# Kernel tuning notes

Hardware: AMD Instinct MI355X
Metric: run time of the kernel (lower is better)

The kernel has to match this reference:

```python
import math
import jax, jax.numpy as jnp
import numpy as np

B, N, F, K = 4, 4096, 128, 32
EPS = 1e-8  # tsl.epsilon
TEMP0, TEMP_DECAY = 1.0, 0.99995


def setup_inputs() -> dict:
    key = jax.random.key(0)
    k1, k2, k3, k4 = jax.random.split(key, 4)
    emb = jax.random.normal(k1, (B, N, F), dtype=jnp.float32)
    adj = jax.random.uniform(k2, (B, N, N), dtype=jnp.float32)
    logits_param = jax.random.normal(k3, (N, K), dtype=jnp.float32)
    u = jax.random.uniform(k4, (B, N, K), dtype=jnp.float32, minval=1e-9, maxval=1.0)
    gumbel_noise = -jnp.log(-jnp.log(u))
    return {"emb": emb, "adj": adj, "logits_param": logits_param, "gumbel_noise": gumbel_noise}


def reference(emb, adj, logits_param, gumbel_noise):
    # temp decays on each get_temp() call in training mode (called twice per forward)
    t1 = max(TEMP0 * TEMP_DECAY, 0.05)
    t2 = max(t1 * TEMP_DECAY, 0.05)

    # ---- gumbel-softmax hard sample with straight-through estimator ----
    y_soft = jax.nn.softmax(logits_param[None] / t1 + gumbel_noise, axis=-1)  # [B,N,K]
    y_hard = jax.nn.one_hot(jnp.argmax(y_soft, axis=-1), K, dtype=y_soft.dtype)
    s_sample = jax.lax.stop_gradient(y_hard - y_soft) + y_soft + EPS  # [B,N,K]

    # ---- soft assignment for regularizers (unbatched [N,K]) ----
    s_soft = jax.nn.softmax(logits_param / t2, axis=-1)  # [N,K]

    # mincut_num = trace(s^T A s) per batch, without forming [K,K]
    As = jnp.einsum('bnm,mk->bnk', adj, s_soft)            # [B,N,K]
    mincut_num = jnp.einsum('nk,bnk->b', s_soft, As)       # [B]
    # mincut_den = trace(s^T D s): D is diag(deg) -> O(N*K) instead of diag_embed
    d_flat = adj.sum(axis=-1)                              # [B,N]
    mincut_den = jnp.einsum('bn,nk,nk->b', d_flat, s_soft, s_soft)
    mincut_loss = -jnp.mean(mincut_num / mincut_den)

    ss = s_soft.T @ s_soft                                 # [K,K]
    ortho_loss = jnp.linalg.norm(ss / jnp.linalg.norm(ss) - jnp.eye(K, dtype=ss.dtype) / math.sqrt(K))

    # ---- pooling ----
    out_emb = jnp.einsum('bnk,bnf->bkf', s_sample, emb)    # [B,K,F]
    As2 = jnp.einsum('bnm,bml->bnl', adj, s_sample)        # [B,N,K]
    out_adj = jnp.einsum('bnk,bnl->bkl', s_sample, As2)    # [B,K,K]

    out_adj = out_adj * (1.0 - jnp.eye(K, dtype=out_adj.dtype))  # zero diagonal
    d = jnp.sqrt(out_adj.sum(axis=-1, keepdims=True)) + EPS
    out_adj = out_adj / d / jnp.swapaxes(d, -1, -2)

    return out_emb, out_adj, s_sample, mincut_loss, ortho_loss
```

## Files before the change

### kernel.cpp

```cpp
#include <hip/hip_runtime.h>
#include <hip/hip_bf16.h>
#include <math.h>

#define B_ 4
#define N_ 4096
#define F_ 128
#define K_ 32
#define EPS_ 1e-8f

typedef __attribute__((ext_vector_type(8))) __bf16 bf16x8;
typedef __attribute__((ext_vector_type(4))) float f32x4;

#define WS_SSOFT   0
#define WS_SQ      131072
#define WS_SS      135168
#define WS_WFS     136192
#define WS_WFH     201728
#define WS_OADJP   463872
#define WS_NUMDEN  1512448
#define WS_PEMB    1514496
#define WS_OADJ    2563072
#define WS_H       2567168

__global__ void k_pre(const float* __restrict__ logits, const float* __restrict__ gum,
                      float* __restrict__ s_soft, float* __restrict__ sq,
                      float* __restrict__ ss, float* __restrict__ s_sample,
                      int* __restrict__ h, bf16x8* __restrict__ wfs,
                      bf16x8* __restrict__ wfh, float t1, float t2) {
  __shared__ float sl[64][33];
  __shared__ int hl[4][64];
  int t = threadIdx.x;
  int r = blockIdx.x;
  int n0 = r * 64;

  if (t < 64) {
    int n = n0 + t;
    float z[32];
    float mx = -1e30f;
    for (int k = 0; k < 32; ++k) { z[k] = logits[n*32+k] / t2; mx = fmaxf(mx, z[k]); }
    float s = 0.f;
    for (int k = 0; k < 32; ++k) { z[k] = expf(z[k]-mx); s += z[k]; }
    float sqa = 0.f;
    for (int k = 0; k < 32; ++k) {
      float v = z[k] / s;
      s_soft[n*32+k] = v;
      sl[t][k] = v;
      sqa += v*v;
    }
    sq[n] = sqa;
  }

  {
    int b = t >> 6, nn = t & 63;
    int n = n0 + nn;
    size_t i = (size_t)b * N_ + n;
    float z[32];
    float mx = -1e30f;
    for (int k = 0; k < 32; ++k) { z[k] = logits[n*32+k]/t1 + gum[i*32+k]; mx = fmaxf(mx, z[k]); }
    float s = 0.f;
    for (int k = 0; k < 32; ++k) { z[k] = expf(z[k]-mx); s += z[k]; }
    int am = 0; float best = -1.f;
    for (int k = 0; k < 32; ++k) { z[k] = z[k]/s; if (z[k] > best) { best = z[k]; am = k; } }
    for (int k = 0; k < 32; ++k) {
      float yh = (k==am) ? 1.f : 0.f;
      s_sample[i*32+k] = (yh - z[k]) + z[k] + EPS_;
    }
    h[i] = am;
    hl[b][nn] = am;
  }
  __syncthreads();

  for (int pp = 0; pp < 4; ++pp) {
    int p = pp*256 + t;
    int k = p >> 5, l = p & 31;
    float a = 0.f;
    for (int rr = 0; rr < 64; ++rr) a += sl[rr][k]*sl[rr][l];
    atomicAdd(&ss[p], a);
  }

  {
    int lane = t & 63;
    int c = (t >> 6) & 1;
    int tts = t >> 7;
    int col = c*16 + (lane & 15);
    int lrow = tts*32 + (lane >> 4)*8;
    bf16x8 v;
    #pragma unroll
    for (int j = 0; j < 8; ++j) v[j] = (__bf16)sl[lrow+j][col];
    wfs[((size_t)(2*r + tts)*2 + c)*64 + lane] = v;
  }

  for (int it = 0; it < 4; ++it) {
    int p = it*256 + t;
    int lane = p & 63;
    int c = (p >> 6) & 1;
    int tts = (p >> 7) & 1;
    int b = p >> 8;
    int cc = c*16 + (lane & 15);
    int lrow = tts*32 + (lane >> 4)*8;
    bf16x8 v;
    #pragma unroll
    for (int j = 0; j < 8; ++j) v[j] = (__bf16)((hl[b][lrow+j] == cc) ? 1.f : 0.f);
    wfh[(((size_t)b*(N_/32) + 2*r + tts)*2 + c)*64 + lane] = v;
  }
}

#define NT(p) __builtin_nontemporal_load((const f32x4*)(p))

__launch_bounds__(256, 4)
__global__ void k_gemm(const float* __restrict__ adj, const bf16x8* __restrict__ wfs,
                       const bf16x8* __restrict__ wfh,
                       const float* __restrict__ s_soft, const float* __restrict__ sq,
                       const int* __restrict__ h, float* __restrict__ numden_p,
                       float* __restrict__ oadjp) {
  __shared__ float oal[1024];
  __shared__ float rn[4], rd[4];
  int t = threadIdx.x;
  int w = t >> 6, l = t & 63;
  int lr = l & 15, lhi = l >> 4;
  int bid = blockIdx.x;
  int sp = bid & 7, r = (bid >> 3) & 31, b = bid >> 8;

  for (int i = t; i < 1024; i += 256) oal[i] = 0.f;
  __syncthreads();

  int row0 = r*128;
  int m0 = sp*512;
  int rowA = row0 + w*32 + lr;

  const float* pA0 = adj + (size_t)b*N_*N_ + (size_t)rowA*N_ + m0 + lhi*8;
  const float* pA1 = pA0 + (size_t)16*N_;
  const bf16x8* pws = wfs + (size_t)(m0 >> 5)*128 + l;
  const bf16x8* pwh = wfh + ((size_t)b*(N_/32) + (m0 >> 5))*128 + l;

  f32x4 acc00 = {0,0,0,0}, acc01 = {0,0,0,0}, acc02 = {0,0,0,0}, acc03 = {0,0,0,0};
  f32x4 acc10 = {0,0,0,0}, acc11 = {0,0,0,0}, acc12 = {0,0,0,0}, acc13 = {0,0,0,0};

  f32x4 a0lo = NT(pA0), a0hi = NT(pA0 + 4);
  f32x4 a1lo = NT(pA1), a1hi = NT(pA1 + 4);
  bf16x8 wc0 = pws[0], wc1 = pws[64], wc2 = pwh[0], wc3 = pwh[64];

  #pragma unroll 1
  for (int c = 0; c < 16; ++c) {
    f32x4 n0lo, n0hi, n1lo, n1hi;
    bf16x8 wn0, wn1, wn2, wn3;
    if (c < 15) {
      pA0 += 32; pA1 += 32; pws += 128; pwh += 128;
      n0lo = NT(pA0); n0hi = NT(pA0 + 4);
      n1lo = NT(pA1); n1hi = NT(pA1 + 4);
      wn0 = pws[0]; wn1 = pws[64]; wn2 = pwh[0]; wn3 = pwh[64];
    }
    bf16x8 fa0, fa1;
    #pragma unroll
    for (int j = 0; j < 4; ++j) {
      fa0[j]   = (__bf16)a0lo[j];
      fa0[j+4] = (__bf16)a0hi[j];
      fa1[j]   = (__bf16)a1lo[j];
      fa1[j+4] = (__bf16)a1hi[j];
    }
    acc00 = __builtin_amdgcn_mfma_f32_16x16x32_bf16(fa0, wc0, acc00, 0, 0, 0);
    acc01 = __builtin_amdgcn_mfma_f32_16x16x32_bf16(fa0, wc1, acc01, 0, 0, 0);
    acc02 = __builtin_amdgcn_mfma_f32_16x16x32_bf16(fa0, wc2, acc02, 0, 0, 0);
    acc03 = __builtin_amdgcn_mfma_f32_16x16x32_bf16(fa0, wc3, acc03, 0, 0, 0);
    acc10 = __builtin_amdgcn_mfma_f32_16x16x32_bf16(fa1, wc0, acc10, 0, 0, 0);
    acc11 = __builtin_amdgcn_mfma_f32_16x16x32_bf16(fa1, wc1, acc11, 0, 0, 0);
    acc12 = __builtin_amdgcn_mfma_f32_16x16x32_bf16(fa1, wc2, acc12, 0, 0, 0);
    acc13 = __builtin_amdgcn_mfma_f32_16x16x32_bf16(fa1, wc3, acc13, 0, 0, 0);
    if (c < 15) {
      a0lo = n0lo; a0hi = n0hi; a1lo = n1lo; a1hi = n1hi;
      wc0 = wn0; wc1 = wn1; wc2 = wn2; wc3 = wn3;
    }
  }

  float numacc = 0.f, denacc = 0.f;
  {
    f32x4 a0s[2] = {acc00, acc10}, a1s[2] = {acc01, acc11};
    f32x4 a2s[2] = {acc02, acc12}, a3s[2] = {acc03, acc13};
    int wrow0 = row0 + w*32;
    #pragma unroll
    for (int rt = 0; rt < 2; ++rt) {
      int rbase = wrow0 + rt*16 + lhi*4;
      #pragma unroll
      for (int i = 0; i < 4; ++i) {
        int row = rbase + i;
        float sqv = sq[row];
        int hv = h[b*N_ + row];
        numacc += a0s[rt][i] * s_soft[row*32 + lr];
        numacc += a1s[rt][i] * s_soft[row*32 + 16 + lr];
        float v2 = a2s[rt][i], v3 = a3s[rt][i];
        denacc += (v2 + v3) * sqv;
        atomicAdd(&oal[hv*32 + lr], v2);
        atomicAdd(&oal[hv*32 + 16 + lr], v3);
      }
    }
  }
  for (int off = 32; off; off >>= 1) {
    numacc += __shfl_down(numacc, off);
    denacc += __shfl_down(denacc, off);
  }
  if (l == 0) { rn[w] = numacc; rd[w] = denacc; }
  __syncthreads();
  if (t == 0) {
    numden_p[bid] = rn[0]+rn[1]+rn[2]+rn[3];
    numden_p[1024 + bid] = rd[0]+rd[1]+rd[2]+rd[3];
  }
  for (int i = t; i < 1024; i += 256) oadjp[(size_t)bid*1024 + i] = oal[i];
}

__global__ void k_outemb(const float* __restrict__ emb, const int* __restrict__ h,
                         float* __restrict__ pemb) {
  __shared__ float accl[32*128];
  int t = threadIdx.x;
  for (int i = t; i < 4096; i += 256) accl[i] = 0.f;
  __syncthreads();
  int b = blockIdx.x >> 6;
  int n0 = (blockIdx.x & 63) * 64;
  int f = t & 127, rr = t >> 7;
  for (int it = 0; it < 32; ++it) {
    int n = n0 + it*2 + rr;
    float v = emb[((size_t)b*N_ + n)*F_ + f];
    int hv = h[b*N_ + n];
    atomicAdd(&accl[hv*128 + f], v);
  }
  __syncthreads();
  for (int i = t; i < 4096; i += 256) pemb[(size_t)blockIdx.x*4096 + i] = accl[i];
}

__global__ void k_reduce(const float* __restrict__ oadjp, const float* __restrict__ pemb,
                         float* __restrict__ oadj, float* __restrict__ out_emb) {
  int blk = blockIdx.x;
  if (blk < 16) {
    int i = blk*256 + threadIdx.x;
    int b = i >> 10, ii = i & 1023;
    float s = 0.f;
    const float* p = oadjp + (size_t)(b*256)*1024 + ii;
    for (int j = 0; j < 256; ++j) s += p[(size_t)j*1024];
    oadj[i] = s;
  } else {
    int i = (blk-16)*256 + threadIdx.x;
    int b = i >> 12, ii = i & 4095;
    float s = 0.f;
    const float* p = pemb + (size_t)(b*64)*4096 + ii;
    for (int j = 0; j < 64; ++j) s += p[(size_t)j*4096];
    out_emb[i] = s;
  }
}

__global__ void k_final(const float* __restrict__ numden_p, const float* __restrict__ oadj,
                        const float* __restrict__ ss, float* __restrict__ dout) {
  __shared__ float dsh[128];
  __shared__ float red[256];
  __shared__ float nd[8];
  int t = threadIdx.x;
  if (t < 8) {
    int b = t & 3;
    const float* p = numden_p + (t >> 2)*1024 + b*256;
    float s = 0.f;
    for (int j = 0; j < 256; ++j) s += p[j];
    nd[t] = s;
  }
  if (t >= 64 && t < 192) {
    int i = t - 64;
    int b = i >> 5, k = i & 31;
    float s = 0.f;
    for (int l = 0; l < 32; ++l) if (l != k) s += oadj[b*1024 + k*32 + l];
    dsh[i] = sqrtf(s) + EPS_;
  }
  __syncthreads();
  for (int i = t; i < 4096; i += 256) {
    int b = i >> 10, k = (i >> 5) & 31, l = i & 31;
    float v = (k == l) ? 0.f : oadj[i] / (dsh[b*32+k] * dsh[b*32+l]);
    dout[16384 + i] = v;
  }
  float a = 0.f;
  for (int i = t; i < 1024; i += 256) { float v = ss[i]; a += v*v; }
  red[t] = a; __syncthreads();
  for (int s2 = 128; s2; s2 >>= 1) { if (t < s2) red[t] += red[t+s2]; __syncthreads(); }
  float fro = sqrtf(red[0]);
  __syncthreads();
  float c = 0.f;
  float inv = 1.f / fro;
  float dk = (float)(1.0 / sqrt(32.0));
  for (int i = t; i < 1024; i += 256) {
    int k = i >> 5, l = i & 31;
    float v = ss[i]*inv - ((k == l) ? dk : 0.f);
    c += v*v;
  }
  red[t] = c; __syncthreads();
  for (int s2 = 128; s2; s2 >>= 1) { if (t < s2) red[t] += red[t+s2]; __syncthreads(); }
  if (t == 0) {
    dout[544769] = sqrtf(red[0]);
    float s = 0.f;
    for (int b = 0; b < 4; ++b) s += nd[b] / nd[4+b];
    dout[544768] = -s*0.25f;
  }
}

extern "C" void kernel_launch(void* const* d_in, const int* in_sizes, int n_in,
                              void* d_out, int out_size, void* d_ws, size_t ws_size,
                              hipStream_t stream) {
  const float* emb    = (const float*)d_in[0];
  const float* adj    = (const float*)d_in[1];
  const float* logits = (const float*)d_in[2];
  const float* gum    = (const float*)d_in[3];
  float* out = (float*)d_out;
  float* ws  = (float*)d_ws;

  float t1 = 0.99995f;
  float t2 = (float)(0.99995 * 0.99995);

  float* s_soft = ws + WS_SSOFT;
  float* sq     = ws + WS_SQ;
  float* ss     = ws + WS_SS;
  bf16x8* wfs   = (bf16x8*)(ws + WS_WFS);
  bf16x8* wfh   = (bf16x8*)(ws + WS_WFH);
  float* oadjp  = ws + WS_OADJP;
  float* ndp    = ws + WS_NUMDEN;
  float* pemb   = ws + WS_PEMB;
  float* oadj   = ws + WS_OADJ;
  int* hbuf     = (int*)(ws + WS_H);

  (void)hipMemsetAsync(ss, 0, 1024 * sizeof(float), stream);

  k_pre   <<<64, 256, 0, stream>>>(logits, gum, s_soft, sq, ss, out + 20480, hbuf, wfs, wfh, t1, t2);
  k_gemm  <<<1024, 256, 0, stream>>>(adj, wfs, wfh, s_soft, sq, hbuf, ndp, oadjp);
  k_outemb<<<256, 256, 0, stream>>>(emb, hbuf, pemb);
  k_reduce<<<80, 256, 0, stream>>>(oadjp, pemb, oadj, out);
  k_final <<<1, 256, 0, stream>>>(ndp, oadj, ss, out);
}
```

Measured before the change: 424.9 us.

## Fuse out_emb into gemm launch and merge reduction/final kernels

The out_emb scatter-accumulate blocks are folded into the gemm kernel as 256 extra leading blocks, and the reduce and final kernels are merged into one post kernel with per-batch blocks. The ss Gram matrix is now written as per-block partials instead of atomics, which removes the memset. This cuts the pipeline from five launches plus a memset to three and should lower launch overhead and tail serialization. The cost is larger shared memory in the gemm kernel (4096 floats), which may reduce occupancy for the gemm blocks.

```diff
diff --git a/kernel.cpp b/kernel.cpp
--- a/kernel.cpp
+++ b/kernel.cpp
@@ -13,18 +13,17 @@
 
 #define WS_SSOFT   0
 #define WS_SQ      131072
-#define WS_SS      135168
-#define WS_WFS     136192
-#define WS_WFH     201728
-#define WS_OADJP   463872
-#define WS_NUMDEN  1512448
-#define WS_PEMB    1514496
-#define WS_OADJ    2563072
-#define WS_H       2567168
+#define WS_SSP     135168
+#define WS_WFS     200704
+#define WS_WFH     266240
+#define WS_OADJP   528384
+#define WS_NUMDEN  1576960
+#define WS_PEMB    1579008
+#define WS_H       2627584
 
 __global__ void k_pre(const float* __restrict__ logits, const float* __restrict__ gum,
                       float* __restrict__ s_soft, float* __restrict__ sq,
-                      float* __restrict__ ss, float* __restrict__ s_sample,
+                      float* __restrict__ ssp, float* __restrict__ s_sample,
                       int* __restrict__ h, bf16x8* __restrict__ wfs,
                       bf16x8* __restrict__ wfh, float t1, float t2) {
   __shared__ float sl[64][33];
@@ -75,7 +74,7 @@
     int k = p >> 5, l = p & 31;
     float a = 0.f;
     for (int rr = 0; rr < 64; ++rr) a += sl[rr][k]*sl[rr][l];
-    atomicAdd(&ss[p], a);
+    ssp[(size_t)r*1024 + p] = a;
   }
 
   {
@@ -108,18 +107,38 @@
 #define NT(p) __builtin_nontemporal_load((const f32x4*)(p))
 
 __launch_bounds__(256, 4)
-__global__ void k_gemm(const float* __restrict__ adj, const bf16x8* __restrict__ wfs,
-                       const bf16x8* __restrict__ wfh,
+__global__ void k_gemm(const float* __restrict__ adj, const float* __restrict__ emb,
+                       const bf16x8* __restrict__ wfs, const bf16x8* __restrict__ wfh,
                        const float* __restrict__ s_soft, const float* __restrict__ sq,
                        const int* __restrict__ h, float* __restrict__ numden_p,
-                       float* __restrict__ oadjp) {
-  __shared__ float oal[1024];
+                       float* __restrict__ oadjp, float* __restrict__ pemb) {
+  __shared__ float sh[4096];
   __shared__ float rn[4], rd[4];
   int t = threadIdx.x;
+  int bid = blockIdx.x;
+
+  if (bid < 256) {
+    for (int i = t; i < 4096; i += 256) sh[i] = 0.f;
+    __syncthreads();
+    int b = bid >> 6;
+    int n0 = (bid & 63) * 64;
+    int f = t & 127, rr = t >> 7;
+    for (int it = 0; it < 32; ++it) {
+      int n = n0 + it*2 + rr;
+      float v = emb[((size_t)b*N_ + n)*F_ + f];
+      int hv = h[b*N_ + n];
+      atomicAdd(&sh[hv*128 + f], v);
+    }
+    __syncthreads();
+    for (int i = t; i < 4096; i += 256) pemb[(size_t)bid*4096 + i] = sh[i];
+    return;
+  }
+
+  int gid = bid - 256;
   int w = t >> 6, l = t & 63;
   int lr = l & 15, lhi = l >> 4;
-  int bid = blockIdx.x;
-  int sp = bid & 7, r = (bid >> 3) & 31, b = bid >> 8;
+  int sp = gid & 7, r = (gid >> 3) & 31, b = gid >> 8;
+  float* oal = sh;
 
   for (int i = t; i < 1024; i += 256) oal[i] = 0.f;
   __syncthreads();
@@ -201,98 +220,86 @@
   if (l == 0) { rn[w] = numacc; rd[w] = denacc; }
   __syncthreads();
   if (t == 0) {
-    numden_p[bid] = rn[0]+rn[1]+rn[2]+rn[3];
-    numden_p[1024 + bid] = rd[0]+rd[1]+rd[2]+rd[3];
-  }
-  for (int i = t; i < 1024; i += 256) oadjp[(size_t)bid*1024 + i] = oal[i];
+    numden_p[gid] = rn[0]+rn[1]+rn[2]+rn[3];
+    numden_p[1024 + gid] = rd[0]+rd[1]+rd[2]+rd[3];
+  }
+  for (int i = t; i < 1024; i += 256) oadjp[(size_t)gid*1024 + i] = oal[i];
 }
 
-__global__ void k_outemb(const float* __restrict__ emb, const int* __restrict__ h,
-                         float* __restrict__ pemb) {
-  __shared__ float accl[32*128];
+__global__ void k_post(const float* __restrict__ oadjp, const float* __restrict__ pemb,
+                       const float* __restrict__ ndp, const float* __restrict__ ssp,
+                       float* __restrict__ dout) {
+  int blk = blockIdx.x;
   int t = threadIdx.x;
-  for (int i = t; i < 4096; i += 256) accl[i] = 0.f;
-  __syncthreads();
-  int b = blockIdx.x >> 6;
-  int n0 = (blockIdx.x & 63) * 64;
-  int f = t & 127, rr = t >> 7;
-  for (int it = 0; it < 32; ++it) {
-    int n = n0 + it*2 + rr;
-    float v = emb[((size_t)b*N_ + n)*F_ + f];
-    int hv = h[b*N_ + n];
-    atomicAdd(&accl[hv*128 + f], v);
-  }
-  __syncthreads();
-  for (int i = t; i < 4096; i += 256) pemb[(size_t)blockIdx.x*4096 + i] = accl[i];
-}
-
-__global__ void k_reduce(const float* __restrict__ oadjp, const float* __restrict__ pemb,
-                         float* __restrict__ oadj, float* __restrict__ out_emb) {
-  int blk = blockIdx.x;
-  if (blk < 16) {
-    int i = blk*256 + threadIdx.x;
-    int b = i >> 10, ii = i & 1023;
-    float s = 0.f;
-    const float* p = oadjp + (size_t)(b*256)*1024 + ii;
-    for (int j = 0; j < 256; ++j) s += p[(size_t)j*1024];
-    oadj[i] = s;
-  } else {
-    int i = (blk-16)*256 + threadIdx.x;
+  if (blk < 64) {
+    int i = blk*256 + t;
     int b = i >> 12, ii = i & 4095;
     float s = 0.f;
     const float* p = pemb + (size_t)(b*64)*4096 + ii;
     for (int j = 0; j < 64; ++j) s += p[(size_t)j*4096];
-    out_emb[i] = s;
-  }
-}
-
-__global__ void k_final(const float* __restrict__ numden_p, const float* __restrict__ oadj,
-                        const float* __restrict__ ss, float* __restrict__ dout) {
-  __shared__ float dsh[128];
-  __shared__ float red[256];
-  __shared__ float nd[8];
-  int t = threadIdx.x;
-  if (t < 8) {
-    int b = t & 3;
-    const float* p = numden_p + (t >> 2)*1024 + b*256;
-    float s = 0.f;
-    for (int j = 0; j < 256; ++j) s += p[j];
-    nd[t] = s;
-  }
-  if (t >= 64 && t < 192) {
-    int i = t - 64;
-    int b = i >> 5, k = i & 31;
-    float s = 0.f;
-    for (int l = 0; l < 32; ++l) if (l != k) s += oadj[b*1024 + k*32 + l];
-    dsh[i] = sqrtf(s) + EPS_;
-  }
-  __syncthreads();
-  for (int i = t; i < 4096; i += 256) {
-    int b = i >> 10, k = (i >> 5) & 31, l = i & 31;
-    float v = (k == l) ? 0.f : oadj[i] / (dsh[b*32+k] * dsh[b*32+l]);
-    dout[16384 + i] = v;
-  }
-  float a = 0.f;
-  for (int i = t; i < 1024; i += 256) { float v = ss[i]; a += v*v; }
-  red[t] = a; __syncthreads();
-  for (int s2 = 128; s2; s2 >>= 1) { if (t < s2) red[t] += red[t+s2]; __syncthreads(); }
-  float fro = sqrtf(red[0]);
-  __syncthreads();
-  float c = 0.f;
-  float inv = 1.f / fro;
-  float dk = (float)(1.0 / sqrt(32.0));
-  for (int i = t; i < 1024; i += 256) {
-    int k = i >> 5, l = i & 31;
-    float v = ss[i]*inv - ((k == l) ? dk : 0.f);
-    c += v*v;
-  }
-  red[t] = c; __syncthreads();
-  for (int s2 = 128; s2; s2 >>= 1) { if (t < s2) red[t] += red[t+s2]; __syncthreads(); }
-  if (t == 0) {
-    dout[544769] = sqrtf(red[0]);
-    float s = 0.f;
-    for (int b = 0; b < 4; ++b) s += nd[b] / nd[4+b];
-    dout[544768] = -s*0.25f;
+    dout[i] = s;
+  } else if (blk < 68) {
+    __shared__ float oal[1024];
+    __shared__ float dsh[32];
+    int b = blk - 64;
+    float a0 = 0.f, a1 = 0.f, a2 = 0.f, a3 = 0.f;
+    const float* p = oadjp + (size_t)b*256*1024 + t;
+    for (int j = 0; j < 256; ++j) {
+      a0 += p[0]; a1 += p[256]; a2 += p[512]; a3 += p[768];
+      p += 1024;
+    }
+    oal[t] = a0; oal[t+256] = a1; oal[t+512] = a2; oal[t+768] = a3;
+    __syncthreads();
+    if (t < 32) {
+      float s = 0.f;
+      for (int l = 0; l < 32; ++l) if (l != t) s += oal[t*32+l];
+      dsh[t] = sqrtf(s) + EPS_;
+    }
+    __syncthreads();
+    for (int i = t; i < 1024; i += 256) {
+      int k = i >> 5, l = i & 31;
+      float v = (k == l) ? 0.f : oal[i] / (dsh[k] * dsh[l]);
+      dout[16384 + b*1024 + i] = v;
+    }
+  } else {
+    __shared__ float red[256];
+    __shared__ float nd[8];
+    if (t < 8) {
+      int b = t & 3;
+      const float* p = ndp + (t >> 2)*1024 + b*256;
+      float s = 0.f;
+      for (int j = 0; j < 256; ++j) s += p[j];
+      nd[t] = s;
+    }
+    float v0 = 0.f, v1 = 0.f, v2 = 0.f, v3 = 0.f;
+    for (int r = 0; r < 64; ++r) {
+      const float* p = ssp + (size_t)r*1024 + t;
+      v0 += p[0]; v1 += p[256]; v2 += p[512]; v3 += p[768];
+    }
+    float a = v0*v0 + v1*v1 + v2*v2 + v3*v3;
+    red[t] = a; __syncthreads();
+    for (int s2 = 128; s2; s2 >>= 1) { if (t < s2) red[t] += red[t+s2]; __syncthreads(); }
+    float fro = sqrtf(red[0]);
+    __syncthreads();
+    float inv = 1.f / fro;
+    float dk = (float)(1.0 / sqrt(32.0));
+    float c = 0.f;
+    {
+      float w;
+      int p0 = t, p1 = t+256, p2 = t+512, p3 = t+768;
+      w = v0*inv - (((p0>>5)==(p0&31)) ? dk : 0.f); c += w*w;
+      w = v1*inv - (((p1>>5)==(p1&31)) ? dk : 0.f); c += w*w;
+      w = v2*inv - (((p2>>5)==(p2&31)) ? dk : 0.f); c += w*w;
+      w = v3*inv - (((p3>>5)==(p3&31)) ? dk : 0.f); c += w*w;
+    }
+    red[t] = c; __syncthreads();
+    for (int s2 = 128; s2; s2 >>= 1) { if (t < s2) red[t] += red[t+s2]; __syncthreads(); }
+    if (t == 0) {
+      dout[544769] = sqrtf(red[0]);
+      float s = 0.f;
+      for (int b = 0; b < 4; ++b) s += nd[b] / nd[4+b];
+      dout[544768] = -s*0.25f;
+    }
   }
 }
 
@@ -311,20 +318,15 @@
 
   float* s_soft = ws + WS_SSOFT;
   float* sq     = ws + WS_SQ;
-  float* ss     = ws + WS_SS;
+  float* ssp    = ws + WS_SSP;
   bf16x8* wfs   = (bf16x8*)(ws + WS_WFS);
   bf16x8* wfh   = (bf16x8*)(ws + WS_WFH);
   float* oadjp  = ws + WS_OADJP;
   float* ndp    = ws + WS_NUMDEN;
   float* pemb   = ws + WS_PEMB;
-  float* oadj   = ws + WS_OADJ;
   int* hbuf     = (int*)(ws + WS_H);
 
-  (void)hipMemsetAsync(ss, 0, 1024 * sizeof(float), stream);
-
-  k_pre   <<<64, 256, 0, stream>>>(logits, gum, s_soft, sq, ss, out + 20480, hbuf, wfs, wfh, t1, t2);
-  k_gemm  <<<1024, 256, 0, stream>>>(adj, wfs, wfh, s_soft, sq, hbuf, ndp, oadjp);
-  k_outemb<<<256, 256, 0, stream>>>(emb, hbuf, pemb);
-  k_reduce<<<80, 256, 0, stream>>>(oadjp, pemb, oadj, out);
-  k_final <<<1, 256, 0, stream>>>(ndp, oadj, ss, out);
+  k_pre  <<<64, 256, 0, stream>>>(logits, gum, s_soft, sq, ssp, out + 20480, hbuf, wfs, wfh, t1, t2);
+  k_gemm <<<1280, 256, 0, stream>>>(adj, emb, wfs, wfh, s_soft, sq, hbuf, ndp, oadjp, pemb);
+  k_post <<<69, 256, 0, stream>>>(oadjp, pemb, ndp, ssp, out);
 }
```

After: 416.8 us. Within noise of the previous version (-1.9%).
